# Performance work log

Measured on AMD Instinct MI355X. Metric: run time of the kernel, lower is better.

## Reference

```python
import jax, jax.numpy as jnp
import numpy as np

N_NODES = 50000
N_EDGES = 800000
F_IN, F_HID, F_OUT = 128, 64, 32


def setup_inputs() -> dict:
    key = jax.random.key(0)
    k1, k2, k3, k4, k5, k6 = jax.random.split(key, 6)
    x = jax.random.normal(k1, (N_NODES, F_IN), dtype=jnp.float32)
    edge_index = jax.random.randint(k2, (2, N_EDGES), 0, N_NODES, dtype=jnp.int64)
    # Glorot-ish init for the two GCNConv linear layers
    W1 = jax.random.normal(k3, (F_IN, F_HID), dtype=jnp.float32) / np.sqrt(F_IN)
    b1 = jnp.zeros((F_HID,), dtype=jnp.float32)
    W2 = jax.random.normal(k4, (F_HID, F_OUT), dtype=jnp.float32) / np.sqrt(F_HID)
    b2 = jnp.zeros((F_OUT,), dtype=jnp.float32)
    return {"x": x, "edge_index": edge_index, "W1": W1, "b1": b1, "W2": W2, "b2": b2}


def _gcn_conv(x, src, dst, norm, W, b):
    # GCNConv: linear transform, then D^{-1/2}(A+I)D^{-1/2} aggregation
    xw = x @ W                                # [N, F_out]
    msg = xw[src] * norm[:, None]             # [E+N, F_out] gather + scale
    out = jax.ops.segment_sum(msg, dst, num_segments=x.shape[0])
    return out + b


def reference(x, edge_index, W1, b1, W2, b2):
    n = x.shape[0]
    self_loops = jnp.arange(n, dtype=edge_index.dtype)
    src = jnp.concatenate([edge_index[0], self_loops])  # [E+N]
    dst = jnp.concatenate([edge_index[1], self_loops])
    # symmetric degree normalization (self-loops guarantee deg >= 1)
    deg = jax.ops.segment_sum(jnp.ones_like(dst, dtype=x.dtype), dst, num_segments=n)
    dinv = jax.lax.rsqrt(deg)
    norm = dinv[src] * dinv[dst]              # [E+N]

    h = _gcn_conv(x, src, dst, norm, W1, b1)
    h = jax.nn.relu(h)
    # dropout p=0.5 is identity in eval mode (training=False)
    out = _gcn_conv(h, src, dst, norm, W2, b2)
    return out
```

## Files before the change

### kernel.cpp

```cpp
#include <hip/hip_runtime.h>
#include <hip/hip_fp16.h>

#define NN 50000
#define NE 800000
#define F_IN 128
#define F_HID 64
#define F_OUT 32
#define CAP 48
#define NBUCK 196
#define BCAP 4500
#define EPB 4096

typedef _Float16 f16x8 __attribute__((ext_vector_type(8)));
typedef float f32x4 __attribute__((ext_vector_type(4)));


__global__ __launch_bounds__(256) void partition_kernel(
        const int* __restrict__ src, const int* __restrict__ dst,
        int* __restrict__ bucket_cnt, unsigned int* __restrict__ bucket_store) {
    __shared__ int hist[NBUCK];
    __shared__ int cur[NBUCK];
    int t = threadIdx.x;
    for (int i = t; i < NBUCK; i += 256) hist[i] = 0;
    __syncthreads();

    int base = blockIdx.x * EPB;
    unsigned int pk[16];
#pragma unroll
    for (int i = 0; i < 16; ++i) {
        int e = base + i * 256 + t;
        if (e < NE) {
            unsigned int d = (unsigned int)dst[e];
            unsigned int s = (unsigned int)src[e];
            pk[i] = (d << 16) | s;
            atomicAdd(&hist[d >> 8], 1);
        } else {
            pk[i] = 0xFFFFFFFFu;
        }
    }
    __syncthreads();

    for (int b = t; b < NBUCK; b += 256) {
        int h = hist[b];
        cur[b] = (h > 0) ? atomicAdd(&bucket_cnt[b], h) : 0;
    }
    __syncthreads();

#pragma unroll
    for (int i = 0; i < 16; ++i) {
        unsigned int p = pk[i];
        if (p != 0xFFFFFFFFu) {
            int b = p >> 24;
            int gpos = atomicAdd(&cur[b], 1);
            if (gpos < BCAP) bucket_store[(size_t)b * BCAP + gpos] = p;
        }
    }
}


__global__ __launch_bounds__(256) void build_slots_kernel(
        const int* __restrict__ bucket_cnt, const unsigned int* __restrict__ bucket_store,
        unsigned short* __restrict__ slot, int* __restrict__ cnt_g, float* __restrict__ dinv) {
    __shared__ unsigned short slot_l[256 * CAP];
    __shared__ int cnt_l[256];
    int t = threadIdx.x;
    int b = blockIdx.x;
    cnt_l[t] = 0;
    __syncthreads();

    int ne = bucket_cnt[b];
    if (ne > BCAP) ne = BCAP;
    const unsigned int* bs = bucket_store + (size_t)b * BCAP;
    for (int j = t; j < ne; j += 256) {
        unsigned int p = bs[j];
        int dl = (p >> 16) & 255;
        int pos = atomicAdd(&cnt_l[dl], 1);
        if (pos < CAP) slot_l[dl * CAP + pos] = (unsigned short)(p & 0xFFFFu);
    }
    __syncthreads();

    unsigned int* sg = (unsigned int*)(slot + (size_t)b * 256 * CAP);
    const unsigned int* sl = (const unsigned int*)slot_l;
    for (int j = t; j < 256 * CAP / 2; j += 256) sg[j] = sl[j];

    int n = b * 256 + t;
    if (n < NN) {
        int c = cnt_l[t];
        cnt_g[n] = c;
        dinv[n] = rsqrtf(1.0f + (float)c);
    }
}


#define XS_STR 136

__global__ __launch_bounds__(256) void xw1_mfma_kernel(
        const float* __restrict__ x, const float* __restrict__ W,
        const float* __restrict__ dinv, __half* __restrict__ outh) {
    __shared__ _Float16 xs[64 * XS_STR];
    __shared__ _Float16 wt[64 * XS_STR];

    int t = threadIdx.x;
    int node0 = blockIdx.x * 64;

    {
        int r = t >> 2;
        int c0 = (t & 3) * 32;
        int gn = node0 + r;
        if (gn > NN - 1) gn = NN - 1;
        const float4* xrow = (const float4*)(x + (size_t)gn * F_IN);
#pragma unroll
        for (int i = 0; i < 8; ++i) {
            float4 v = xrow[(c0 >> 2) + i];
            _Float16* p = &xs[r * XS_STR + c0 + i * 4];
            p[0] = (_Float16)v.x; p[1] = (_Float16)v.y;
            p[2] = (_Float16)v.z; p[3] = (_Float16)v.w;
        }
    }
#pragma unroll
    for (int i = 0; i < 8; ++i) {
        int idx4 = t + i * 256;
        int k = idx4 >> 4;
        int n0 = (idx4 & 15) << 2;
        float4 v = ((const float4*)W)[idx4];
        wt[(n0 + 0) * XS_STR + k] = (_Float16)v.x;
        wt[(n0 + 1) * XS_STR + k] = (_Float16)v.y;
        wt[(n0 + 2) * XS_STR + k] = (_Float16)v.z;
        wt[(n0 + 3) * XS_STR + k] = (_Float16)v.w;
    }
    __syncthreads();

    int wave = t >> 6;
    int l = t & 63;
    int quad = l >> 4;
    int lm = l & 15;

    f32x4 acc[4] = {{0,0,0,0},{0,0,0,0},{0,0,0,0},{0,0,0,0}};
    const _Float16* abase = &xs[(wave * 16 + lm) * XS_STR + quad * 8];
#pragma unroll
    for (int kk4 = 0; kk4 < 4; ++kk4) {
        int kk = kk4 * 32;
        f16x8 a = *(const f16x8*)(abase + kk);
#pragma unroll
        for (int ft = 0; ft < 4; ++ft) {
            f16x8 b = *(const f16x8*)&wt[(ft * 16 + lm) * XS_STR + kk + quad * 8];
            acc[ft] = __builtin_amdgcn_mfma_f32_16x16x32_f16(a, b, acc[ft], 0, 0, 0);
        }
    }

    __syncthreads();
    float di[4];
#pragma unroll
    for (int r = 0; r < 4; ++r) {
        int gn = node0 + wave * 16 + quad * 4 + r;
        if (gn > NN - 1) gn = NN - 1;
        di[r] = dinv[gn];
    }
    _Float16* ot = xs;
#pragma unroll
    for (int ft = 0; ft < 4; ++ft) {
#pragma unroll
        for (int r = 0; r < 4; ++r) {
            int row_l = wave * 16 + quad * 4 + r;
            ot[row_l * 64 + ft * 16 + lm] = (_Float16)(acc[ft][r] * di[r]);
        }
    }
    __syncthreads();
#pragma unroll
    for (int i = 0; i < 2; ++i) {
        int idx = t + i * 256;
        int row = idx >> 3;
        int c8 = (idx & 7) * 8;
        int gn = node0 + row;
        if (gn < NN)
            *(uint4*)(outh + (size_t)gn * 64 + c8) = *(const uint4*)&ot[row * 64 + c8];
    }
}


__global__ __launch_bounds__(256) void hw2_tiled_kernel(
        const __half* __restrict__ h, const float* __restrict__ W,
        const float* __restrict__ dinv, __half* __restrict__ outh) {
    __shared__ float4 xs4[F_HID * 32];
    __shared__ float4 wl4[F_HID * 8];
    float* xs = (float*)xs4;
    float* wl = (float*)wl4;

    int t = threadIdx.x;
    int node0 = blockIdx.x * 128;

    for (int i = t; i < F_HID * 8; i += 256) wl4[i] = ((const float4*)W)[i];

    {
        int node = t & 127;
        int gn = node0 + node;
        if (gn > NN - 1) gn = NN - 1;
        const uint2* hrow = (const uint2*)(h + (size_t)gn * F_HID);
        int kh = t >> 7;
        for (int r = 0; r < 8; ++r) {
            int kq = r * 2 + kh;
            uint2 u = hrow[kq];
            __half2 p0 = *(__half2*)&u.x;
            __half2 p1 = *(__half2*)&u.y;
            float2 f0 = __half22float2(p0);
            float2 f1 = __half22float2(p1);
            int k = kq * 4;
            xs[(k + 0) * 128 + node] = f0.x;
            xs[(k + 1) * 128 + node] = f0.y;
            xs[(k + 2) * 128 + node] = f1.x;
            xs[(k + 3) * 128 + node] = f1.y;
        }
    }
    __syncthreads();

    int fq = t & 7;
    int nq = t >> 3;
    float4 a0 = {0,0,0,0}, a1 = {0,0,0,0}, a2 = {0,0,0,0}, a3 = {0,0,0,0};
#pragma unroll 8
    for (int k = 0; k < F_HID; ++k) {
        float4 xv = *(const float4*)&xs[k * 128 + nq * 4];
        float4 wv = *(const float4*)&wl[k * 32 + fq * 4];
        a0.x += xv.x * wv.x; a0.y += xv.x * wv.y; a0.z += xv.x * wv.z; a0.w += xv.x * wv.w;
        a1.x += xv.y * wv.x; a1.y += xv.y * wv.y; a1.z += xv.y * wv.z; a1.w += xv.y * wv.w;
        a2.x += xv.z * wv.x; a2.y += xv.z * wv.y; a2.z += xv.z * wv.z; a2.w += xv.z * wv.w;
        a3.x += xv.w * wv.x; a3.y += xv.w * wv.y; a3.z += xv.w * wv.z; a3.w += xv.w * wv.w;
    }

    float4 acc[4] = {a0, a1, a2, a3};
#pragma unroll
    for (int i = 0; i < 4; ++i) {
        int n = node0 + nq * 4 + i;
        if (n < NN) {
            float di = dinv[n];
            __half2* op = (__half2*)(outh + (size_t)n * F_OUT + fq * 4);
            op[0] = __floats2half2_rn(acc[i].x * di, acc[i].y * di);
            op[1] = __floats2half2_rn(acc[i].z * di, acc[i].w * di);
        }
    }
}


__global__ void gather64_kernel(const __half* __restrict__ scaled,
                                const int* __restrict__ cnt,
                                const unsigned short* __restrict__ slot,
                                const float* __restrict__ dinv,
                                const float* __restrict__ bias,
                                __half* __restrict__ outh) {
    int lane = threadIdx.x & 63;
    int n = blockIdx.x * 4 + (threadIdx.x >> 6);
    if (n >= NN) return;
    int st = lane >> 4;
    int fl4 = lane & 15;
    const uint2* base = (const uint2*)scaled;
    int deg = cnt[n];
    if (deg > CAP) deg = CAP;
    const unsigned short* srow = slot + (size_t)n * CAP;
    float a0 = 0, a1 = 0, a2 = 0, a3 = 0;
    int e = st;
    for (; e + 4 < deg; e += 8) {
        int s0 = srow[e];
        int s1 = srow[e + 4];
        uint2 u0 = base[(size_t)s0 * 16 + fl4];
        uint2 u1 = base[(size_t)s1 * 16 + fl4];
        float2 p0 = __half22float2(*(__half2*)&u0.x);
        float2 p1 = __half22float2(*(__half2*)&u0.y);
        float2 q0 = __half22float2(*(__half2*)&u1.x);
        float2 q1 = __half22float2(*(__half2*)&u1.y);
        a0 += p0.x + q0.x; a1 += p0.y + q0.y;
        a2 += p1.x + q1.x; a3 += p1.y + q1.y;
    }
    for (; e < deg; e += 4) {
        int s = srow[e];
        uint2 u = base[(size_t)s * 16 + fl4];
        float2 p0 = __half22float2(*(__half2*)&u.x);
        float2 p1 = __half22float2(*(__half2*)&u.y);
        a0 += p0.x; a1 += p0.y; a2 += p1.x; a3 += p1.y;
    }
    a0 += __shfl_xor(a0, 16, 64); a1 += __shfl_xor(a1, 16, 64);
    a2 += __shfl_xor(a2, 16, 64); a3 += __shfl_xor(a3, 16, 64);
    a0 += __shfl_xor(a0, 32, 64); a1 += __shfl_xor(a1, 32, 64);
    a2 += __shfl_xor(a2, 32, 64); a3 += __shfl_xor(a3, 32, 64);
    if (st == 0) {
        uint2 u = base[(size_t)n * 16 + fl4];
        float2 s0 = __half22float2(*(__half2*)&u.x);
        float2 s1 = __half22float2(*(__half2*)&u.y);
        float4 b4 = ((const float4*)bias)[fl4];
        float di = dinv[n];
        float v0 = di * (a0 + s0.x) + b4.x;
        float v1 = di * (a1 + s0.y) + b4.y;
        float v2 = di * (a2 + s1.x) + b4.z;
        float v3 = di * (a3 + s1.y) + b4.w;
        v0 = v0 > 0.f ? v0 : 0.f; v1 = v1 > 0.f ? v1 : 0.f;
        v2 = v2 > 0.f ? v2 : 0.f; v3 = v3 > 0.f ? v3 : 0.f;
        uint2 o;
        *(__half2*)&o.x = __floats2half2_rn(v0, v1);
        *(__half2*)&o.y = __floats2half2_rn(v2, v3);
        ((uint2*)outh)[(size_t)n * 16 + fl4] = o;
    }
}

__global__ void gather32_kernel(const __half* __restrict__ scaled,
                                const int* __restrict__ cnt,
                                const unsigned short* __restrict__ slot,
                                const float* __restrict__ dinv,
                                const float* __restrict__ bias,
                                float* __restrict__ out) {
    int lane = threadIdx.x & 63;
    int n = blockIdx.x * 4 + (threadIdx.x >> 6);
    if (n >= NN) return;
    int st = lane >> 3;
    int fl4 = lane & 7;
    const uint2* base = (const uint2*)scaled;
    int deg = cnt[n];
    if (deg > CAP) deg = CAP;
    const unsigned short* srow = slot + (size_t)n * CAP;
    float a0 = 0, a1 = 0, a2 = 0, a3 = 0;
    int e = st;
    for (; e + 8 < deg; e += 16) {
        int s0 = srow[e];
        int s1 = srow[e + 8];
        uint2 u0 = base[(size_t)s0 * 8 + fl4];
        uint2 u1 = base[(size_t)s1 * 8 + fl4];
        float2 p0 = __half22float2(*(__half2*)&u0.x);
        float2 p1 = __half22float2(*(__half2*)&u0.y);
        float2 q0 = __half22float2(*(__half2*)&u1.x);
        float2 q1 = __half22float2(*(__half2*)&u1.y);
        a0 += p0.x + q0.x; a1 += p0.y + q0.y;
        a2 += p1.x + q1.x; a3 += p1.y + q1.y;
    }
    for (; e < deg; e += 8) {
        int s = srow[e];
        uint2 u = base[(size_t)s * 8 + fl4];
        float2 p0 = __half22float2(*(__half2*)&u.x);
        float2 p1 = __half22float2(*(__half2*)&u.y);
        a0 += p0.x; a1 += p0.y; a2 += p1.x; a3 += p1.y;
    }
    a0 += __shfl_xor(a0, 8, 64);  a1 += __shfl_xor(a1, 8, 64);
    a2 += __shfl_xor(a2, 8, 64);  a3 += __shfl_xor(a3, 8, 64);
    a0 += __shfl_xor(a0, 16, 64); a1 += __shfl_xor(a1, 16, 64);
    a2 += __shfl_xor(a2, 16, 64); a3 += __shfl_xor(a3, 16, 64);
    a0 += __shfl_xor(a0, 32, 64); a1 += __shfl_xor(a1, 32, 64);
    a2 += __shfl_xor(a2, 32, 64); a3 += __shfl_xor(a3, 32, 64);
    if (st == 0) {
        uint2 u = base[(size_t)n * 8 + fl4];
        float2 s0 = __half22float2(*(__half2*)&u.x);
        float2 s1 = __half22float2(*(__half2*)&u.y);
        float4 b4 = ((const float4*)bias)[fl4];
        float di = dinv[n];
        float4 r;
        r.x = di * (a0 + s0.x) + b4.x;
        r.y = di * (a1 + s0.y) + b4.y;
        r.z = di * (a2 + s1.x) + b4.z;
        r.w = di * (a3 + s1.y) + b4.w;
        ((float4*)out)[(size_t)n * 8 + fl4] = r;
    }
}


extern "C" void kernel_launch(void* const* d_in, const int* in_sizes, int n_in,
                              void* d_out, int out_size, void* d_ws, size_t ws_size,
                              hipStream_t stream) {
    const float* x  = (const float*)d_in[0];
    const int*   ei = (const int*)d_in[1];
    const float* W1 = (const float*)d_in[2];
    const float* b1 = (const float*)d_in[3];
    const float* W2 = (const float*)d_in[4];
    const float* b2 = (const float*)d_in[5];
    const int* src = ei;
    const int* dst = ei + NE;

    float*          ws      = (float*)d_ws;
    float*          dinv    = ws;
    int*            cnt     = (int*)(ws + 50048);
    int*            bcnt    = (int*)(ws + 100096);
    unsigned int*   bstore  = (unsigned int*)(ws + 100352);
    unsigned short* slot    = (unsigned short*)(ws + 982352);
    __half*         xw1h    = (__half*)(ws + 2186576);
    __half*         h       = xw1h + (size_t)NN * F_HID;
    __half*         hw2h    = xw1h;
    float*          out     = (float*)d_out;

    hipMemsetAsync(bcnt, 0, NBUCK * sizeof(int), stream);
    partition_kernel<<<(NE + EPB - 1) / EPB, 256, 0, stream>>>(src, dst, bcnt, bstore);
    build_slots_kernel<<<NBUCK, 256, 0, stream>>>(bcnt, bstore, slot, cnt, dinv);

    xw1_mfma_kernel<<<(NN + 63) / 64, 256, 0, stream>>>(x, W1, dinv, xw1h);
    gather64_kernel<<<(NN + 3) / 4, 256, 0, stream>>>(xw1h, cnt, slot, dinv, b1, h);

    hw2_tiled_kernel<<<(NN + 127) / 128, 256, 0, stream>>>(h, W2, dinv, hw2h);
    gather32_kernel<<<(NN + 3) / 4, 256, 0, stream>>>(hw2h, cnt, slot, dinv, b2, out);
}
```

Baseline: 164.9 us.

## Fuse partition with XW1 GEMM, fuse layer-2 linear into gather, drop memset

Edge partitioning and the first dense transform now run as one launch, with the two halves assigned to different block ranges. The dinv scaling moves out of the GEMM and into the gather, so the GEMM no longer depends on degree computation. Partitioning writes per-block, per-bucket cells with count transposes instead of global atomics, which removes the memset, and build_slots reads those cells back. The layer-1 gather now computes relu(h) in shared memory and multiplies by W2 directly, which removes the separate hw2 kernel and the h round trip. The tradeoffs are per-edge dinv lookups in the gather, a serial per-cell loop in build_slots, and overflow if a cell exceeds 64 edges.

```diff
diff --git a/kernel.cpp b/kernel.cpp
--- a/kernel.cpp
+++ b/kernel.cpp
@@ -8,100 +8,63 @@
 #define F_OUT 32
 #define CAP 48
 #define NBUCK 196
-#define BCAP 4500
 #define EPB 4096
+#define CELL 64
+#define NXW1 782
 
 typedef _Float16 f16x8 __attribute__((ext_vector_type(8)));
 typedef float f32x4 __attribute__((ext_vector_type(4)));
-
-
-__global__ __launch_bounds__(256) void partition_kernel(
+#define XS_STR 136
+
+
+__global__ __launch_bounds__(256) void fused_xw1_partition_kernel(
+        const float* __restrict__ x, const float* __restrict__ W,
         const int* __restrict__ src, const int* __restrict__ dst,
-        int* __restrict__ bucket_cnt, unsigned int* __restrict__ bucket_store) {
+        int* __restrict__ cnt2t, unsigned int* __restrict__ bstore2,
+        __half* __restrict__ outh) {
+    __shared__ _Float16 xs[64 * XS_STR];
+    __shared__ _Float16 wt[64 * XS_STR];
     __shared__ int hist[NBUCK];
     __shared__ int cur[NBUCK];
     int t = threadIdx.x;
-    for (int i = t; i < NBUCK; i += 256) hist[i] = 0;
-    __syncthreads();
-
-    int base = blockIdx.x * EPB;
-    unsigned int pk[16];
-#pragma unroll
-    for (int i = 0; i < 16; ++i) {
-        int e = base + i * 256 + t;
-        if (e < NE) {
-            unsigned int d = (unsigned int)dst[e];
-            unsigned int s = (unsigned int)src[e];
-            pk[i] = (d << 16) | s;
-            atomicAdd(&hist[d >> 8], 1);
-        } else {
-            pk[i] = 0xFFFFFFFFu;
-        }
-    }
-    __syncthreads();
-
-    for (int b = t; b < NBUCK; b += 256) {
-        int h = hist[b];
-        cur[b] = (h > 0) ? atomicAdd(&bucket_cnt[b], h) : 0;
-    }
-    __syncthreads();
-
-#pragma unroll
-    for (int i = 0; i < 16; ++i) {
-        unsigned int p = pk[i];
-        if (p != 0xFFFFFFFFu) {
-            int b = p >> 24;
-            int gpos = atomicAdd(&cur[b], 1);
-            if (gpos < BCAP) bucket_store[(size_t)b * BCAP + gpos] = p;
-        }
-    }
-}
-
-
-__global__ __launch_bounds__(256) void build_slots_kernel(
-        const int* __restrict__ bucket_cnt, const unsigned int* __restrict__ bucket_store,
-        unsigned short* __restrict__ slot, int* __restrict__ cnt_g, float* __restrict__ dinv) {
-    __shared__ unsigned short slot_l[256 * CAP];
-    __shared__ int cnt_l[256];
-    int t = threadIdx.x;
-    int b = blockIdx.x;
-    cnt_l[t] = 0;
-    __syncthreads();
-
-    int ne = bucket_cnt[b];
-    if (ne > BCAP) ne = BCAP;
-    const unsigned int* bs = bucket_store + (size_t)b * BCAP;
-    for (int j = t; j < ne; j += 256) {
-        unsigned int p = bs[j];
-        int dl = (p >> 16) & 255;
-        int pos = atomicAdd(&cnt_l[dl], 1);
-        if (pos < CAP) slot_l[dl * CAP + pos] = (unsigned short)(p & 0xFFFFu);
-    }
-    __syncthreads();
-
-    unsigned int* sg = (unsigned int*)(slot + (size_t)b * 256 * CAP);
-    const unsigned int* sl = (const unsigned int*)slot_l;
-    for (int j = t; j < 256 * CAP / 2; j += 256) sg[j] = sl[j];
-
-    int n = b * 256 + t;
-    if (n < NN) {
-        int c = cnt_l[t];
-        cnt_g[n] = c;
-        dinv[n] = rsqrtf(1.0f + (float)c);
-    }
-}
-
-
-#define XS_STR 136
-
-__global__ __launch_bounds__(256) void xw1_mfma_kernel(
-        const float* __restrict__ x, const float* __restrict__ W,
-        const float* __restrict__ dinv, __half* __restrict__ outh) {
-    __shared__ _Float16 xs[64 * XS_STR];
-    __shared__ _Float16 wt[64 * XS_STR];
-
-    int t = threadIdx.x;
-    int node0 = blockIdx.x * 64;
+
+    if (blockIdx.x < NBUCK) {
+        int blk = blockIdx.x;
+        for (int i = t; i < NBUCK; i += 256) hist[i] = 0;
+        __syncthreads();
+        int base = blk * EPB;
+        unsigned int pk[16];
+#pragma unroll
+        for (int i = 0; i < 16; ++i) {
+            int e = base + i * 256 + t;
+            if (e < NE) {
+                unsigned int d = (unsigned int)dst[e];
+                unsigned int s = (unsigned int)src[e];
+                pk[i] = (d << 16) | s;
+                atomicAdd(&hist[d >> 8], 1);
+            } else {
+                pk[i] = 0xFFFFFFFFu;
+            }
+        }
+        __syncthreads();
+        for (int b = t; b < NBUCK; b += 256) {
+            cur[b] = 0;
+            cnt2t[b * NBUCK + blk] = hist[b];
+        }
+        __syncthreads();
+#pragma unroll
+        for (int i = 0; i < 16; ++i) {
+            unsigned int p = pk[i];
+            if (p != 0xFFFFFFFFu) {
+                int b = p >> 24;
+                int pos = atomicAdd(&cur[b], 1);
+                if (pos < CELL) bstore2[((size_t)blk * NBUCK + b) * CELL + pos] = p;
+            }
+        }
+        return;
+    }
+
+    int node0 = (blockIdx.x - NBUCK) * 64;
 
     {
         int r = t >> 2;
@@ -149,20 +112,13 @@
     }
 
     __syncthreads();
-    float di[4];
-#pragma unroll
-    for (int r = 0; r < 4; ++r) {
-        int gn = node0 + wave * 16 + quad * 4 + r;
-        if (gn > NN - 1) gn = NN - 1;
-        di[r] = dinv[gn];
-    }
     _Float16* ot = xs;
 #pragma unroll
     for (int ft = 0; ft < 4; ++ft) {
 #pragma unroll
         for (int r = 0; r < 4; ++r) {
             int row_l = wave * 16 + quad * 4 + r;
-            ot[row_l * 64 + ft * 16 + lm] = (_Float16)(acc[ft][r] * di[r]);
+            ot[row_l * 64 + ft * 16 + lm] = (_Float16)acc[ft][r];
         }
     }
     __syncthreads();
@@ -178,80 +134,59 @@
 }
 
 
-__global__ __launch_bounds__(256) void hw2_tiled_kernel(
-        const __half* __restrict__ h, const float* __restrict__ W,
-        const float* __restrict__ dinv, __half* __restrict__ outh) {
-    __shared__ float4 xs4[F_HID * 32];
-    __shared__ float4 wl4[F_HID * 8];
-    float* xs = (float*)xs4;
-    float* wl = (float*)wl4;
-
+__global__ __launch_bounds__(256) void build_slots_kernel(
+        const int* __restrict__ cnt2t, const unsigned int* __restrict__ bstore2,
+        unsigned short* __restrict__ slot, int* __restrict__ cnt_g, float* __restrict__ dinv) {
+    __shared__ unsigned short slot_l[256 * CAP];
+    __shared__ int cnt_l[256];
     int t = threadIdx.x;
-    int node0 = blockIdx.x * 128;
-
-    for (int i = t; i < F_HID * 8; i += 256) wl4[i] = ((const float4*)W)[i];
-
-    {
-        int node = t & 127;
-        int gn = node0 + node;
-        if (gn > NN - 1) gn = NN - 1;
-        const uint2* hrow = (const uint2*)(h + (size_t)gn * F_HID);
-        int kh = t >> 7;
-        for (int r = 0; r < 8; ++r) {
-            int kq = r * 2 + kh;
-            uint2 u = hrow[kq];
-            __half2 p0 = *(__half2*)&u.x;
-            __half2 p1 = *(__half2*)&u.y;
-            float2 f0 = __half22float2(p0);
-            float2 f1 = __half22float2(p1);
-            int k = kq * 4;
-            xs[(k + 0) * 128 + node] = f0.x;
-            xs[(k + 1) * 128 + node] = f0.y;
-            xs[(k + 2) * 128 + node] = f1.x;
-            xs[(k + 3) * 128 + node] = f1.y;
-        }
-    }
-    __syncthreads();
-
-    int fq = t & 7;
-    int nq = t >> 3;
-    float4 a0 = {0,0,0,0}, a1 = {0,0,0,0}, a2 = {0,0,0,0}, a3 = {0,0,0,0};
-#pragma unroll 8
-    for (int k = 0; k < F_HID; ++k) {
-        float4 xv = *(const float4*)&xs[k * 128 + nq * 4];
-        float4 wv = *(const float4*)&wl[k * 32 + fq * 4];
-        a0.x += xv.x * wv.x; a0.y += xv.x * wv.y; a0.z += xv.x * wv.z; a0.w += xv.x * wv.w;
-        a1.x += xv.y * wv.x; a1.y += xv.y * wv.y; a1.z += xv.y * wv.z; a1.w += xv.y * wv.w;
-        a2.x += xv.z * wv.x; a2.y += xv.z * wv.y; a2.z += xv.z * wv.z; a2.w += xv.z * wv.w;
-        a3.x += xv.w * wv.x; a3.y += xv.w * wv.y; a3.z += xv.w * wv.z; a3.w += xv.w * wv.w;
-    }
-
-    float4 acc[4] = {a0, a1, a2, a3};
-#pragma unroll
-    for (int i = 0; i < 4; ++i) {
-        int n = node0 + nq * 4 + i;
-        if (n < NN) {
-            float di = dinv[n];
-            __half2* op = (__half2*)(outh + (size_t)n * F_OUT + fq * 4);
-            op[0] = __floats2half2_rn(acc[i].x * di, acc[i].y * di);
-            op[1] = __floats2half2_rn(acc[i].z * di, acc[i].w * di);
-        }
-    }
-}
-
-
-__global__ void gather64_kernel(const __half* __restrict__ scaled,
-                                const int* __restrict__ cnt,
-                                const unsigned short* __restrict__ slot,
-                                const float* __restrict__ dinv,
-                                const float* __restrict__ bias,
-                                __half* __restrict__ outh) {
-    int lane = threadIdx.x & 63;
-    int n = blockIdx.x * 4 + (threadIdx.x >> 6);
-    if (n >= NN) return;
+    int b = blockIdx.x;
+    cnt_l[t] = 0;
+    __syncthreads();
+
+    for (int blk = t; blk < NBUCK; blk += 256) {
+        int c = cnt2t[b * NBUCK + blk];
+        if (c > CELL) c = CELL;
+        const unsigned int* seg = bstore2 + ((size_t)blk * NBUCK + b) * CELL;
+        for (int j = 0; j < c; ++j) {
+            unsigned int p = seg[j];
+            int dl = (p >> 16) & 255;
+            int pos = atomicAdd(&cnt_l[dl], 1);
+            if (pos < CAP) slot_l[dl * CAP + pos] = (unsigned short)(p & 0xFFFFu);
+        }
+    }
+    __syncthreads();
+
+    unsigned int* sg = (unsigned int*)(slot + (size_t)b * 256 * CAP);
+    const unsigned int* sl = (const unsigned int*)slot_l;
+    for (int j = t; j < 256 * CAP / 2; j += 256) sg[j] = sl[j];
+
+    int n = b * 256 + t;
+    if (n < NN) {
+        int c = cnt_l[t];
+        cnt_g[n] = c;
+        dinv[n] = rsqrtf(1.0f + (float)c);
+    }
+}
+
+
+__global__ __launch_bounds__(256) void gather64_w2_kernel(
+        const __half* __restrict__ xw, const int* __restrict__ cnt,
+        const unsigned short* __restrict__ slot, const float* __restrict__ dinv,
+        const float* __restrict__ b1, const float* __restrict__ W2,
+        __half* __restrict__ hw2h) {
+    __shared__ float w2s[F_HID * F_OUT];
+    __shared__ float hl[4][F_HID];
+    int t = threadIdx.x;
+    for (int i = t; i < F_HID * F_OUT / 4; i += 256)
+        ((float4*)w2s)[i] = ((const float4*)W2)[i];
+
+    int lane = t & 63;
+    int wv = t >> 6;
+    int n = blockIdx.x * 4 + wv;
     int st = lane >> 4;
     int fl4 = lane & 15;
-    const uint2* base = (const uint2*)scaled;
+    const uint2* base = (const uint2*)xw;
     int deg = cnt[n];
     if (deg > CAP) deg = CAP;
     const unsigned short* srow = slot + (size_t)n * CAP;
@@ -260,51 +195,64 @@
     for (; e + 4 < deg; e += 8) {
         int s0 = srow[e];
         int s1 = srow[e + 4];
+        float dv0 = dinv[s0], dv1 = dinv[s1];
         uint2 u0 = base[(size_t)s0 * 16 + fl4];
         uint2 u1 = base[(size_t)s1 * 16 + fl4];
         float2 p0 = __half22float2(*(__half2*)&u0.x);
         float2 p1 = __half22float2(*(__half2*)&u0.y);
         float2 q0 = __half22float2(*(__half2*)&u1.x);
         float2 q1 = __half22float2(*(__half2*)&u1.y);
-        a0 += p0.x + q0.x; a1 += p0.y + q0.y;
-        a2 += p1.x + q1.x; a3 += p1.y + q1.y;
+        a0 += dv0 * p0.x + dv1 * q0.x;
+        a1 += dv0 * p0.y + dv1 * q0.y;
+        a2 += dv0 * p1.x + dv1 * q1.x;
+        a3 += dv0 * p1.y + dv1 * q1.y;
     }
     for (; e < deg; e += 4) {
         int s = srow[e];
+        float dv = dinv[s];
         uint2 u = base[(size_t)s * 16 + fl4];
         float2 p0 = __half22float2(*(__half2*)&u.x);
         float2 p1 = __half22float2(*(__half2*)&u.y);
-        a0 += p0.x; a1 += p0.y; a2 += p1.x; a3 += p1.y;
+        a0 += dv * p0.x; a1 += dv * p0.y; a2 += dv * p1.x; a3 += dv * p1.y;
     }
     a0 += __shfl_xor(a0, 16, 64); a1 += __shfl_xor(a1, 16, 64);
     a2 += __shfl_xor(a2, 16, 64); a3 += __shfl_xor(a3, 16, 64);
     a0 += __shfl_xor(a0, 32, 64); a1 += __shfl_xor(a1, 32, 64);
     a2 += __shfl_xor(a2, 32, 64); a3 += __shfl_xor(a3, 32, 64);
     if (st == 0) {
+        float di = dinv[n];
         uint2 u = base[(size_t)n * 16 + fl4];
         float2 s0 = __half22float2(*(__half2*)&u.x);
         float2 s1 = __half22float2(*(__half2*)&u.y);
-        float4 b4 = ((const float4*)bias)[fl4];
-        float di = dinv[n];
-        float v0 = di * (a0 + s0.x) + b4.x;
-        float v1 = di * (a1 + s0.y) + b4.y;
-        float v2 = di * (a2 + s1.x) + b4.z;
-        float v3 = di * (a3 + s1.y) + b4.w;
-        v0 = v0 > 0.f ? v0 : 0.f; v1 = v1 > 0.f ? v1 : 0.f;
-        v2 = v2 > 0.f ? v2 : 0.f; v3 = v3 > 0.f ? v3 : 0.f;
-        uint2 o;
-        *(__half2*)&o.x = __floats2half2_rn(v0, v1);
-        *(__half2*)&o.y = __floats2half2_rn(v2, v3);
-        ((uint2*)outh)[(size_t)n * 16 + fl4] = o;
-    }
-}
-
-__global__ void gather32_kernel(const __half* __restrict__ scaled,
-                                const int* __restrict__ cnt,
-                                const unsigned short* __restrict__ slot,
-                                const float* __restrict__ dinv,
-                                const float* __restrict__ bias,
-                                float* __restrict__ out) {
+        float4 bb = ((const float4*)b1)[fl4];
+        float v0 = di * (a0 + di * s0.x) + bb.x;
+        float v1 = di * (a1 + di * s0.y) + bb.y;
+        float v2 = di * (a2 + di * s1.x) + bb.z;
+        float v3 = di * (a3 + di * s1.y) + bb.w;
+        float* hr = &hl[wv][fl4 * 4];
+        hr[0] = v0 > 0.f ? v0 : 0.f;
+        hr[1] = v1 > 0.f ? v1 : 0.f;
+        hr[2] = v2 > 0.f ? v2 : 0.f;
+        hr[3] = v3 > 0.f ? v3 : 0.f;
+    }
+    __syncthreads();
+    if (t < 128) {
+        int nq = t >> 5;
+        int f = t & 31;
+        int gn = blockIdx.x * 4 + nq;
+        const float* hr = hl[nq];
+        float acc = 0.0f;
+#pragma unroll 16
+        for (int k = 0; k < F_HID; ++k) acc += hr[k] * w2s[k * F_OUT + f];
+        hw2h[(size_t)gn * F_OUT + f] = __float2half(acc * dinv[gn]);
+    }
+}
+
+
+__global__ __launch_bounds__(256) void gather32_kernel(
+        const __half* __restrict__ scaled, const int* __restrict__ cnt,
+        const unsigned short* __restrict__ slot, const float* __restrict__ dinv,
+        const float* __restrict__ bias, float* __restrict__ out) {
     int lane = threadIdx.x & 63;
     int n = blockIdx.x * 4 + (threadIdx.x >> 6);
     if (n >= NN) return;
@@ -372,21 +320,16 @@
     float*          ws      = (float*)d_ws;
     float*          dinv    = ws;
     int*            cnt     = (int*)(ws + 50048);
-    int*            bcnt    = (int*)(ws + 100096);
-    unsigned int*   bstore  = (unsigned int*)(ws + 100352);
-    unsigned short* slot    = (unsigned short*)(ws + 982352);
-    __half*         xw1h    = (__half*)(ws + 2186576);
-    __half*         h       = xw1h + (size_t)NN * F_HID;
-    __half*         hw2h    = xw1h;
+    int*            cnt2t   = (int*)(ws + 100096);
+    unsigned int*   bstore2 = (unsigned int*)(ws + 138624);
+    unsigned short* slot    = (unsigned short*)(ws + 2597248);
+    __half*         xw1h    = (__half*)(ws + 3801472);
+    __half*         hw2h    = (__half*)(ws + 5401472);
     float*          out     = (float*)d_out;
 
-    hipMemsetAsync(bcnt, 0, NBUCK * sizeof(int), stream);
-    partition_kernel<<<(NE + EPB - 1) / EPB, 256, 0, stream>>>(src, dst, bcnt, bstore);
-    build_slots_kernel<<<NBUCK, 256, 0, stream>>>(bcnt, bstore, slot, cnt, dinv);
-
-    xw1_mfma_kernel<<<(NN + 63) / 64, 256, 0, stream>>>(x, W1, dinv, xw1h);
-    gather64_kernel<<<(NN + 3) / 4, 256, 0, stream>>>(xw1h, cnt, slot, dinv, b1, h);
-
-    hw2_tiled_kernel<<<(NN + 127) / 128, 256, 0, stream>>>(h, W2, dinv, hw2h);
-    gather32_kernel<<<(NN + 3) / 4, 256, 0, stream>>>(hw2h, cnt, slot, dinv, b2, out);
-}
+    fused_xw1_partition_kernel<<<NBUCK + NXW1, 256, 0, stream>>>(
+        x, W1, src, dst, cnt2t, bstore2, xw1h);
+    build_slots_kernel<<<NBUCK, 256, 0, stream>>>(cnt2t, bstore2, slot, cnt, dinv);
+    gather64_w2_kernel<<<NN / 4, 256, 0, stream>>>(xw1h, cnt, slot, dinv, b1, W2, hw2h);
+    gather32_kernel<<<NN / 4, 256, 0, stream>>>(hw2h, cnt, slot, dinv, b2, out);
+}
```

After: 154.1 us. 1.07x faster.
